# Kernel optimization log

Hardware: AMD Instinct MI355X
Metric: run time of the kernel (lower is better)

Reference implementation:

```python
import jax, jax.numpy as jnp
import numpy as np

SEQ, B, D_IN, D_H = 1024, 64, 256, 256


def setup_inputs() -> dict:
    key = jax.random.key(0)
    ks = jax.random.split(key, 9)
    scale = 1.0 / np.sqrt(D_IN + D_H)
    inputs = jax.random.normal(ks[0], (SEQ, B, D_IN), dtype=jnp.float32)
    def lin(k):
        kw, kb = jax.random.split(k)
        W = jax.random.uniform(kw, (D_IN + D_H, D_H), jnp.float32, -scale, scale)
        b = jax.random.uniform(kb, (D_H,), jnp.float32, -scale, scale)
        return W, b
    Wf, bf = lin(ks[1])
    Wi, bi = lin(ks[2])
    Wg, bg = lin(ks[3])
    Wo, bo = lin(ks[4])
    return {"inputs": inputs, "Wf": Wf, "bf": bf, "Wi": Wi, "bi": bi,
            "Wg": Wg, "bg": bg, "Wo": Wo, "bo": bo}


def reference(inputs, Wf, bf, Wi, bi, Wg, bg, Wo, bo):
    B_ = inputs.shape[1]
    hx0 = jnp.zeros((B_, D_H), dtype=inputs.dtype)
    cx0 = jnp.zeros((B_, D_H), dtype=inputs.dtype)

    def step(carry, x):
        hx, cx = carry
        comb = jnp.concatenate([x, hx], axis=1)  # [B, D_IN + D_H]
        f = jax.nn.sigmoid(comb @ Wf + bf)
        i = jax.nn.sigmoid(comb @ Wi + bi)
        g = jnp.tanh(comb @ Wg + bg)
        o = jax.nn.sigmoid(comb @ Wo + bo)
        cx = f * cx + i * g
        hx = o * jnp.tanh(cx)
        return (hx, cx), hx

    (hx, cx), outputs = jax.lax.scan(step, (hx0, cx0), inputs)
    return outputs, hx, cx
```

## Files before the change

kernel.cpp:

```cpp
#include <hip/hip_runtime.h>
#include <hip/hip_bf16.h>


typedef _Float16 f16;
typedef _Float16 f16x4 __attribute__((ext_vector_type(4)));
typedef _Float16 f16x8 __attribute__((ext_vector_type(8)));
typedef float f32x4 __attribute__((ext_vector_type(4)));
typedef int i32x4 __attribute__((ext_vector_type(4)));

#define SEQ 1024
#define BATCH 64
#define DIN 256
#define DH 256
#define NCOL 1024

#define WXP_OFF   0u
#define WHQ_OFF   524288u
#define SCL_OFF   786432u
#define BIAS_OFF  790528u
#define HXS8_OFF  794624u
#define CXS_OFF   811008u
#define SMX_OFF   876544u
#define XP_OFF    880640u

__device__ __forceinline__ float fast_sigmoid(float x) {
  float e = __expf(-x);
  return __builtin_amdgcn_rcpf(1.0f + e);
}
__device__ __forceinline__ float fast_tanh(float x) {
  x = fminf(fmaxf(x, -15.0f), 15.0f);
  float e = __expf(2.0f * x);
  return (e - 1.0f) * __builtin_amdgcn_rcpf(e + 1.0f);
}
__device__ __forceinline__ void lds_barrier() {
  asm volatile("s_waitcnt lgkmcnt(0)\n\ts_barrier" ::: "memory");
}
__device__ __forceinline__ i32x4 MQ(i32x4 a, i32x4 b, i32x4 c) {
  return __builtin_amdgcn_mfma_i32_16x16x64_i8(a, b, c, 0, 0, 0);
}

__global__ void qlstm_prep(const float* __restrict__ Wf, const float* __restrict__ Wi,
                           const float* __restrict__ Wg, const float* __restrict__ Wo,
                           const float* __restrict__ bf_, const float* __restrict__ bi_,
                           const float* __restrict__ bg_, const float* __restrict__ bo_,
                           f16* __restrict__ Wxp, float* __restrict__ biasp,
                           int* __restrict__ smx) {
  int tid = blockIdx.x * 256 + threadIdx.x;
  if (tid < 4 * 256 * 256) {
    int g = tid >> 16;
    int rem = tid & 65535;
    int k = rem >> 8, n = rem & 255;
    const float* W = (g == 0) ? Wf : (g == 1) ? Wi : (g == 2) ? Wg : Wo;
    float v = W[k * 256 + n];
    int j = n * 4 + g;
    Wxp[((size_t)(k >> 3) * 1024 + j) * 8 + (k & 7)] = (f16)v;
  }
  if (tid < 1024) {
    int g = tid >> 8, n = tid & 255;
    const float* bb = (g == 0) ? bf_ : (g == 1) ? bi_ : (g == 2) ? bg_ : bo_;
    biasp[n * 4 + g] = bb[n];
    smx[tid] = 0;
  }
}

__global__ __launch_bounds__(256) void qlstm_prepmax(
    const float* __restrict__ Wf, const float* __restrict__ Wi,
    const float* __restrict__ Wg, const float* __restrict__ Wo,
    int* __restrict__ smx) {
  int bk = blockIdx.x;
  int g = bk & 3, r0 = (bk >> 2) * 32;
  int n = threadIdx.x;
  const float* W = (g == 0) ? Wf : (g == 1) ? Wi : (g == 2) ? Wg : Wo;
  float pm = 0.0f;
  for (int r = 0; r < 32; ++r)
    pm = fmaxf(pm, fabsf(W[(size_t)(256 + r0 + r) * 256 + n]));
  atomicMax(&smx[g * 256 + n], __float_as_int(pm));
}

__global__ __launch_bounds__(256) void qlstm_prepq(
    const float* __restrict__ Wf, const float* __restrict__ Wi,
    const float* __restrict__ Wg, const float* __restrict__ Wo,
    const int* __restrict__ smx, char* __restrict__ WhQ, float* __restrict__ scl) {
  int bk = blockIdx.x;
  int g = bk & 3, r = bk >> 2;
  int n = threadIdx.x;
  const float* W = (g == 0) ? Wf : (g == 1) ? Wi : (g == 2) ? Wg : Wo;
  float mx = __int_as_float(smx[g * 256 + n]);
  float s = (mx > 0.0f) ? mx * (1.0f / 127.0f) : 1.0f;
  float v = W[(size_t)(256 + r) * 256 + n];
  int q = (int)rintf(v * (1.0f / s));
  q = q > 127 ? 127 : (q < -127 ? -127 : q);
  int w = n >> 4, c = n & 15;
  int kt = r >> 6, kp = r & 63;
  int lane = (kp >> 4) * 16 + c, jj = kp & 15;
  WhQ[((size_t)((w * 16 + g * 4 + kt) * 64 + lane)) * 16 + jj] = (char)q;
  if (r == 0) scl[g * 256 + n] = s * (1.0f / 127.0f);
}

__global__ __launch_bounds__(256) void qlstm_xproj(
    const float* __restrict__ X, const f16* __restrict__ Wxp,
    const float* __restrict__ biasp, f16* __restrict__ Xp2) {
  __shared__ f16 As[128][72];
  __shared__ f16 Bs[8 * 128 * 8];

  int tid = threadIdx.x;
  int tm = blockIdx.x, tn = blockIdx.y;
  int wave = tid >> 6, lane = tid & 63;
  int qm = (wave & 1) * 64, qn = (wave >> 1) * 64;
  int lm = lane & 15, lk = lane >> 4;

  f32x4 acc[4][4];
#pragma unroll
  for (int a = 0; a < 4; ++a)
#pragma unroll
    for (int b = 0; b < 4; ++b) acc[a][b] = (f32x4)0.0f;

  for (int k0 = 0; k0 < 256; k0 += 64) {
    {
      int r = tid >> 1, c0 = (tid & 1) * 32;
      const float4* src = (const float4*)(X + (size_t)(tm * 128 + r) * 256 + k0 + c0);
#pragma unroll
      for (int i = 0; i < 8; ++i) {
        float4 v = src[i];
        f16x4 pk = {(f16)v.x, (f16)v.y, (f16)v.z, (f16)v.w};
        *(f16x4*)&As[r][c0 + i * 4] = pk;
      }
    }
    {
#pragma unroll
      for (int it = 0; it < 4; ++it) {
        int idx = it * 256 + tid;
        int kgi = idx >> 7, n = idx & 127;
        ((uint4*)Bs)[idx] =
            *(const uint4*)(Wxp + (((size_t)(k0 >> 3) + kgi) * 1024 + tn * 128 + n) * 8);
      }
    }
    __syncthreads();
#pragma unroll
    for (int ks = 0; ks < 2; ++ks) {
      f16x8 af[4], bfr[4];
#pragma unroll
      for (int mi = 0; mi < 4; ++mi)
        af[mi] = *(const f16x8*)&As[qm + mi * 16 + lm][ks * 32 + lk * 8];
#pragma unroll
      for (int ni = 0; ni < 4; ++ni)
        bfr[ni] = *(const f16x8*)&Bs[(((ks * 4 + lk) * 128) + qn + ni * 16 + lm) * 8];
#pragma unroll
      for (int mi = 0; mi < 4; ++mi)
#pragma unroll
        for (int ni = 0; ni < 4; ++ni)
          acc[mi][ni] = __builtin_amdgcn_mfma_f32_16x16x32_f16(af[mi], bfr[ni],
                                                               acc[mi][ni], 0, 0, 0);
    }
    __syncthreads();
  }
  int m0 = tm * 128 + qm, j0 = tn * 128 + qn;
#pragma unroll
  for (int mi = 0; mi < 4; ++mi)
#pragma unroll
    for (int ni = 0; ni < 4; ++ni) {
      int j = j0 + ni * 16 + lm;
      float bv = biasp[j];
#pragma unroll
      for (int r = 0; r < 4; ++r) {
        int m = m0 + mi * 16 + lk * 4 + r;
        Xp2[(size_t)m * 1024 + j] = (f16)(acc[mi][ni][r] + bv);
      }
    }
}

__global__ __launch_bounds__(1024, 4) void qlstm_seq(
    const f16* __restrict__ Xp2, const i32x4* __restrict__ WhQ,
    const float* __restrict__ scl,
    float* __restrict__ out, char* __restrict__ hxs8, float* __restrict__ cxs,
    float* __restrict__ hxout, float* __restrict__ cxout, int t0, int t1) {
  __shared__ char hxq[2][256];

  int tid = threadIdx.x;
  int wv = tid >> 6, lane = tid & 63, c = lane & 15;
  int b = blockIdx.x;
  int h = wv * 16 + c;

  i32x4 wq[4][4];
  {
    const i32x4* wp = WhQ + (size_t)(wv * 16) * 64 + lane;
#pragma unroll
    for (int g = 0; g < 4; ++g)
#pragma unroll
      for (int kt = 0; kt < 4; ++kt) wq[g][kt] = wp[(g * 4 + kt) * 64];
  }
  float sc[4];
#pragma unroll
  for (int g = 0; g < 4; ++g) sc[g] = scl[g * 256 + h];

  int par0 = t0 & 1;
  if (tid < 16) {
    uint4 v;
    if (t0 == 0) v = uint4{0u, 0u, 0u, 0u};
    else v = ((const uint4*)(hxs8 + (size_t)b * 256))[tid];
    *(uint4*)(&hxq[par0][tid * 16]) = v;
  }
  float cx = (t0 != 0) ? cxs[(size_t)b * 256 + h] : 0.0f;

  __syncthreads();

  int koff = (lane >> 4) << 4;
  float hv = 0.0f;
  for (int t = t0; t < t1; ++t) {
    int par = t & 1, parn = par ^ 1;
    const char* hp = &hxq[par][0];

    uint2 xr = *(const uint2*)(Xp2 + (((size_t)(t - t0) * BATCH + b) * 256 + h) * 4);

    i32x4 a0 = *(const i32x4*)(hp + koff);
    i32x4 a1 = *(const i32x4*)(hp + 64 + koff);
    i32x4 a2 = *(const i32x4*)(hp + 128 + koff);
    i32x4 a3 = *(const i32x4*)(hp + 192 + koff);

    i32x4 acc0{}, acc1{}, acc2{}, acc3{};
    acc0 = MQ(a0, wq[0][0], acc0); acc1 = MQ(a0, wq[1][0], acc1);
    acc2 = MQ(a0, wq[2][0], acc2); acc3 = MQ(a0, wq[3][0], acc3);
    acc0 = MQ(a1, wq[0][1], acc0); acc1 = MQ(a1, wq[1][1], acc1);
    acc2 = MQ(a1, wq[2][1], acc2); acc3 = MQ(a1, wq[3][1], acc3);
    acc0 = MQ(a2, wq[0][2], acc0); acc1 = MQ(a2, wq[1][2], acc1);
    acc2 = MQ(a2, wq[2][2], acc2); acc3 = MQ(a2, wq[3][2], acc3);
    acc0 = MQ(a3, wq[0][3], acc0); acc1 = MQ(a3, wq[1][3], acc1);
    acc2 = MQ(a3, wq[2][3], acc2); acc3 = MQ(a3, wq[3][3], acc3);

    f16x4 xh = __builtin_bit_cast(f16x4, xr);
    float p0 = fmaf((float)acc0[0], sc[0], (float)xh[0]);
    float p1 = fmaf((float)acc1[0], sc[1], (float)xh[1]);
    float p2 = fmaf((float)acc2[0], sc[2], (float)xh[2]);
    float p3 = fmaf((float)acc3[0], sc[3], (float)xh[3]);

    float vf = fast_sigmoid(p0);
    float vi = fast_sigmoid(p1);
    float vg = fast_tanh(p2);
    float vo = fast_sigmoid(p3);
    cx = fmaf(vf, cx, vi * vg);
    hv = vo * fast_tanh(cx);

    if (lane < 16) {
      hxq[parn][h] = (char)(int)rintf(hv * 127.0f);
      out[((size_t)t * BATCH + b) * 256 + h] = hv;
    }
    lds_barrier();
  }

  if (tid < 16)
    ((uint4*)(hxs8 + (size_t)b * 256))[tid] = *(const uint4*)(&hxq[t1 & 1][tid * 16]);
  if (lane < 16) {
    cxs[(size_t)b * 256 + h] = cx;
    if (t1 == SEQ) {
      hxout[(size_t)b * 256 + h] = hv;
      cxout[(size_t)b * 256 + h] = cx;
    }
  }
}

extern "C" void kernel_launch(void* const* d_in, const int* in_sizes, int n_in,
                              void* d_out, int out_size, void* d_ws, size_t ws_size,
                              hipStream_t stream) {
  const float* X  = (const float*)d_in[0];
  const float* Wf = (const float*)d_in[1]; const float* bf_ = (const float*)d_in[2];
  const float* Wi = (const float*)d_in[3]; const float* bi_ = (const float*)d_in[4];
  const float* Wg = (const float*)d_in[5]; const float* bg_ = (const float*)d_in[6];
  const float* Wo = (const float*)d_in[7]; const float* bo_ = (const float*)d_in[8];
  float* out = (float*)d_out;

  char* ws = (char*)d_ws;
  f16*   Wxp   = (f16*)(ws + WXP_OFF);
  char*  WhQ   = (char*)(ws + WHQ_OFF);
  float* scl   = (float*)(ws + SCL_OFF);
  float* biasp = (float*)(ws + BIAS_OFF);
  char*  hxs8  = (char*)(ws + HXS8_OFF);
  float* cxs   = (float*)(ws + CXS_OFF);
  int*   smx   = (int*)(ws + SMX_OFF);
  f16*   Xp2   = (f16*)(ws + XP_OFF);

  size_t avail = (ws_size > XP_OFF) ? (ws_size - XP_OFF) : 0;
  int Tc = SEQ;
  while (Tc > 2 && (size_t)Tc * BATCH * NCOL * 2 > avail) Tc >>= 1;

  qlstm_prep<<<1024, 256, 0, stream>>>(Wf, Wi, Wg, Wo, bf_, bi_, bg_, bo_,
                                       Wxp, biasp, smx);
  qlstm_prepmax<<<32, 256, 0, stream>>>(Wf, Wi, Wg, Wo, smx);
  qlstm_prepq<<<1024, 256, 0, stream>>>(Wf, Wi, Wg, Wo, smx, WhQ, scl);

  float* hxout = out + (size_t)SEQ * BATCH * DH;
  float* cxout = hxout + BATCH * DH;

  for (int t0 = 0; t0 < SEQ; t0 += Tc) {
    dim3 g1(Tc * BATCH / 128, NCOL / 128);
    qlstm_xproj<<<g1, 256, 0, stream>>>(X + (size_t)t0 * BATCH * DIN, Wxp, biasp, Xp2);
    qlstm_seq<<<BATCH, 1024, 0, stream>>>(Xp2, (const i32x4*)WhQ, scl, out, hxs8, cxs,
                                          hxout, cxout, t0, t0 + Tc);
  }
}
```

Measured before the change: 1.161 ms.

## Restructure input projection to load X once per block, fuse weight-scale prep kernels

The input-projection GEMM now loads and converts each 128-row X tile once into a padded LDS buffer covering the full K=256, then loops over all 8 output column tiles, staging full-K weight tiles in dynamic LDS. This replaces the 2D grid where each block reloaded X per column tile. The weight max-reduction and int8 quantization kernels are merged into one kernel that reduces in shared memory instead of using global atomics, and tanh drops its clamp and uses a cheaper formula. The trade-offs are fewer xproj blocks (lower parallelism), about 128KB of LDS per block, and possible tanh edge behavior for large inputs.

```diff
diff --git a/kernel.cpp b/kernel.cpp
--- a/kernel.cpp
+++ b/kernel.cpp
@@ -20,17 +20,17 @@
 #define BIAS_OFF  790528u
 #define HXS8_OFF  794624u
 #define CXS_OFF   811008u
-#define SMX_OFF   876544u
-#define XP_OFF    880640u
+#define XP_OFF    876544u
+
+#define XPROJ_LDS 131584
 
 __device__ __forceinline__ float fast_sigmoid(float x) {
   float e = __expf(-x);
   return __builtin_amdgcn_rcpf(1.0f + e);
 }
 __device__ __forceinline__ float fast_tanh(float x) {
-  x = fminf(fmaxf(x, -15.0f), 15.0f);
   float e = __expf(2.0f * x);
-  return (e - 1.0f) * __builtin_amdgcn_rcpf(e + 1.0f);
+  return fmaf(-2.0f, __builtin_amdgcn_rcpf(e + 1.0f), 1.0f);
 }
 __device__ __forceinline__ void lds_barrier() {
   asm volatile("s_waitcnt lgkmcnt(0)\n\ts_barrier" ::: "memory");
@@ -43,8 +43,7 @@
                            const float* __restrict__ Wg, const float* __restrict__ Wo,
                            const float* __restrict__ bf_, const float* __restrict__ bi_,
                            const float* __restrict__ bg_, const float* __restrict__ bo_,
-                           f16* __restrict__ Wxp, float* __restrict__ biasp,
-                           int* __restrict__ smx) {
+                           f16* __restrict__ Wxp, float* __restrict__ biasp) {
   int tid = blockIdx.x * 256 + threadIdx.x;
   if (tid < 4 * 256 * 256) {
     int g = tid >> 16;
@@ -59,114 +58,118 @@
     int g = tid >> 8, n = tid & 255;
     const float* bb = (g == 0) ? bf_ : (g == 1) ? bi_ : (g == 2) ? bg_ : bo_;
     biasp[n * 4 + g] = bb[n];
-    smx[tid] = 0;
-  }
-}
-
-__global__ __launch_bounds__(256) void qlstm_prepmax(
+  }
+}
+
+__global__ __launch_bounds__(1024) void qlstm_prepq(
     const float* __restrict__ Wf, const float* __restrict__ Wi,
     const float* __restrict__ Wg, const float* __restrict__ Wo,
-    int* __restrict__ smx) {
-  int bk = blockIdx.x;
-  int g = bk & 3, r0 = (bk >> 2) * 32;
-  int n = threadIdx.x;
+    char* __restrict__ WhQ, float* __restrict__ scl) {
+  __shared__ float red[4][256];
+  int g = blockIdx.x;
+  int tid = threadIdx.x, q = tid >> 8, n = tid & 255;
   const float* W = (g == 0) ? Wf : (g == 1) ? Wi : (g == 2) ? Wg : Wo;
+
   float pm = 0.0f;
-  for (int r = 0; r < 32; ++r)
-    pm = fmaxf(pm, fabsf(W[(size_t)(256 + r0 + r) * 256 + n]));
-  atomicMax(&smx[g * 256 + n], __float_as_int(pm));
-}
-
-__global__ __launch_bounds__(256) void qlstm_prepq(
-    const float* __restrict__ Wf, const float* __restrict__ Wi,
-    const float* __restrict__ Wg, const float* __restrict__ Wo,
-    const int* __restrict__ smx, char* __restrict__ WhQ, float* __restrict__ scl) {
-  int bk = blockIdx.x;
-  int g = bk & 3, r = bk >> 2;
-  int n = threadIdx.x;
-  const float* W = (g == 0) ? Wf : (g == 1) ? Wi : (g == 2) ? Wg : Wo;
-  float mx = __int_as_float(smx[g * 256 + n]);
+  for (int r = 0; r < 64; ++r)
+    pm = fmaxf(pm, fabsf(W[(size_t)(256 + q * 64 + r) * 256 + n]));
+  red[q][n] = pm;
+  __syncthreads();
+  float mx = fmaxf(fmaxf(red[0][n], red[1][n]), fmaxf(red[2][n], red[3][n]));
   float s = (mx > 0.0f) ? mx * (1.0f / 127.0f) : 1.0f;
-  float v = W[(size_t)(256 + r) * 256 + n];
-  int q = (int)rintf(v * (1.0f / s));
-  q = q > 127 ? 127 : (q < -127 ? -127 : q);
+  float inv = 1.0f / s;
+
   int w = n >> 4, c = n & 15;
-  int kt = r >> 6, kp = r & 63;
-  int lane = (kp >> 4) * 16 + c, jj = kp & 15;
-  WhQ[((size_t)((w * 16 + g * 4 + kt) * 64 + lane)) * 16 + jj] = (char)q;
-  if (r == 0) scl[g * 256 + n] = s * (1.0f / 127.0f);
+  for (int rr = 0; rr < 64; ++rr) {
+    int r = q * 64 + rr;
+    float v = W[(size_t)(256 + r) * 256 + n];
+    int qv = (int)rintf(v * inv);
+    qv = qv > 127 ? 127 : (qv < -127 ? -127 : qv);
+    int kt = r >> 6, kp = r & 63;
+    int lane = (kp >> 4) * 16 + c, jj = kp & 15;
+    WhQ[((size_t)((w * 16 + g * 4 + kt) * 64 + lane)) * 16 + jj] = (char)qv;
+  }
+  if (q == 0) scl[g * 256 + n] = s * (1.0f / 127.0f);
 }
 
 __global__ __launch_bounds__(256) void qlstm_xproj(
     const float* __restrict__ X, const f16* __restrict__ Wxp,
     const float* __restrict__ biasp, f16* __restrict__ Xp2) {
-  __shared__ f16 As[128][72];
-  __shared__ f16 Bs[8 * 128 * 8];
+  extern __shared__ char smem[];
+  f16* As = (f16*)smem;
+  f16* Bs = (f16*)(smem + 66048);
 
   int tid = threadIdx.x;
-  int tm = blockIdx.x, tn = blockIdx.y;
+  int tm = blockIdx.x;
   int wave = tid >> 6, lane = tid & 63;
   int qm = (wave & 1) * 64, qn = (wave >> 1) * 64;
   int lm = lane & 15, lk = lane >> 4;
 
-  f32x4 acc[4][4];
-#pragma unroll
-  for (int a = 0; a < 4; ++a)
-#pragma unroll
-    for (int b = 0; b < 4; ++b) acc[a][b] = (f32x4)0.0f;
-
-  for (int k0 = 0; k0 < 256; k0 += 64) {
+  {
+    int r = tid >> 1, c0 = (tid & 1) * 128;
+    const float4* src = (const float4*)(X + (size_t)(tm * 128 + r) * 256 + c0);
+#pragma unroll
+    for (int i = 0; i < 32; ++i) {
+      float4 v = src[i];
+      f16x4 pk = {(f16)v.x, (f16)v.y, (f16)v.z, (f16)v.w};
+      *(f16x4*)&As[r * 258 + c0 + i * 4] = pk;
+    }
+  }
+
+  for (int tn = 0; tn < 8; ++tn) {
+    __syncthreads();
     {
-      int r = tid >> 1, c0 = (tid & 1) * 32;
-      const float4* src = (const float4*)(X + (size_t)(tm * 128 + r) * 256 + k0 + c0);
-#pragma unroll
-      for (int i = 0; i < 8; ++i) {
-        float4 v = src[i];
-        f16x4 pk = {(f16)v.x, (f16)v.y, (f16)v.z, (f16)v.w};
-        *(f16x4*)&As[r][c0 + i * 4] = pk;
+#pragma unroll
+      for (int it = 0; it < 16; ++it) {
+        int idx = it * 256 + tid;
+        int kg = idx >> 7, n = idx & 127;
+        ((uint4*)Bs)[idx] =
+            *(const uint4*)(Wxp + ((size_t)kg * 1024 + tn * 128 + n) * 8);
       }
     }
-    {
-#pragma unroll
-      for (int it = 0; it < 4; ++it) {
-        int idx = it * 256 + tid;
-        int kgi = idx >> 7, n = idx & 127;
-        ((uint4*)Bs)[idx] =
-            *(const uint4*)(Wxp + (((size_t)(k0 >> 3) + kgi) * 1024 + tn * 128 + n) * 8);
+    __syncthreads();
+
+    f32x4 acc[4][4];
+#pragma unroll
+    for (int a = 0; a < 4; ++a)
+#pragma unroll
+      for (int b = 0; b < 4; ++b) acc[a][b] = (f32x4)0.0f;
+
+#pragma unroll
+    for (int k0 = 0; k0 < 256; k0 += 64) {
+#pragma unroll
+      for (int ks = 0; ks < 2; ++ks) {
+        f16x8 af[4], bfr[4];
+        int kgab = (k0 >> 3) + ks * 4 + lk;
+#pragma unroll
+        for (int mi = 0; mi < 4; ++mi)
+          af[mi] = *(const f16x8*)&As[(qm + mi * 16 + lm) * 258 + k0 + ks * 32 + lk * 8];
+#pragma unroll
+        for (int ni = 0; ni < 4; ++ni)
+          bfr[ni] = *(const f16x8*)&Bs[((size_t)kgab * 128 + qn + ni * 16 + lm) * 8];
+#pragma unroll
+        for (int mi = 0; mi < 4; ++mi)
+#pragma unroll
+          for (int ni = 0; ni < 4; ++ni)
+            acc[mi][ni] = __builtin_amdgcn_mfma_f32_16x16x32_f16(af[mi], bfr[ni],
+                                                                 acc[mi][ni], 0, 0, 0);
       }
     }
-    __syncthreads();
-#pragma unroll
-    for (int ks = 0; ks < 2; ++ks) {
-      f16x8 af[4], bfr[4];
-#pragma unroll
-      for (int mi = 0; mi < 4; ++mi)
-        af[mi] = *(const f16x8*)&As[qm + mi * 16 + lm][ks * 32 + lk * 8];
-#pragma unroll
-      for (int ni = 0; ni < 4; ++ni)
-        bfr[ni] = *(const f16x8*)&Bs[(((ks * 4 + lk) * 128) + qn + ni * 16 + lm) * 8];
-#pragma unroll
-      for (int mi = 0; mi < 4; ++mi)
-#pragma unroll
-        for (int ni = 0; ni < 4; ++ni)
-          acc[mi][ni] = __builtin_amdgcn_mfma_f32_16x16x32_f16(af[mi], bfr[ni],
-                                                               acc[mi][ni], 0, 0, 0);
-    }
-    __syncthreads();
-  }
-  int m0 = tm * 128 + qm, j0 = tn * 128 + qn;
-#pragma unroll
-  for (int mi = 0; mi < 4; ++mi)
-#pragma unroll
-    for (int ni = 0; ni < 4; ++ni) {
-      int j = j0 + ni * 16 + lm;
-      float bv = biasp[j];
-#pragma unroll
-      for (int r = 0; r < 4; ++r) {
-        int m = m0 + mi * 16 + lk * 4 + r;
-        Xp2[(size_t)m * 1024 + j] = (f16)(acc[mi][ni][r] + bv);
+
+    int m0 = tm * 128 + qm, j0 = tn * 128 + qn;
+#pragma unroll
+    for (int mi = 0; mi < 4; ++mi)
+#pragma unroll
+      for (int ni = 0; ni < 4; ++ni) {
+        int j = j0 + ni * 16 + lm;
+        float bv = biasp[j];
+#pragma unroll
+        for (int r = 0; r < 4; ++r) {
+          int m = m0 + mi * 16 + lk * 4 + r;
+          Xp2[(size_t)m * 1024 + j] = (f16)(acc[mi][ni][r] + bv);
+        }
       }
-    }
+  }
 }
 
 __global__ __launch_bounds__(1024, 4) void qlstm_seq(
@@ -275,7 +278,6 @@
   float* biasp = (float*)(ws + BIAS_OFF);
   char*  hxs8  = (char*)(ws + HXS8_OFF);
   float* cxs   = (float*)(ws + CXS_OFF);
-  int*   smx   = (int*)(ws + SMX_OFF);
   f16*   Xp2   = (f16*)(ws + XP_OFF);
 
   size_t avail = (ws_size > XP_OFF) ? (ws_size - XP_OFF) : 0;
@@ -283,16 +285,19 @@
   while (Tc > 2 && (size_t)Tc * BATCH * NCOL * 2 > avail) Tc >>= 1;
 
   qlstm_prep<<<1024, 256, 0, stream>>>(Wf, Wi, Wg, Wo, bf_, bi_, bg_, bo_,
-                                       Wxp, biasp, smx);
-  qlstm_prepmax<<<32, 256, 0, stream>>>(Wf, Wi, Wg, Wo, smx);
-  qlstm_prepq<<<1024, 256, 0, stream>>>(Wf, Wi, Wg, Wo, smx, WhQ, scl);
+                                       Wxp, biasp);
+  qlstm_prepq<<<4, 1024, 0, stream>>>(Wf, Wi, Wg, Wo, WhQ, scl);
+
+  (void)hipFuncSetAttribute((const void*)qlstm_xproj,
+                            hipFuncAttributeMaxDynamicSharedMemorySize,
+                            XPROJ_LDS);
 
   float* hxout = out + (size_t)SEQ * BATCH * DH;
   float* cxout = hxout + BATCH * DH;
 
   for (int t0 = 0; t0 < SEQ; t0 += Tc) {
-    dim3 g1(Tc * BATCH / 128, NCOL / 128);
-    qlstm_xproj<<<g1, 256, 0, stream>>>(X + (size_t)t0 * BATCH * DIN, Wxp, biasp, Xp2);
+    qlstm_xproj<<<Tc * 64 / 128, 256, XPROJ_LDS, stream>>>(
+        X + (size_t)t0 * BATCH * DIN, Wxp, biasp, Xp2);
     qlstm_seq<<<BATCH, 1024, 0, stream>>>(Xp2, (const i32x4*)WhQ, scl, out, hxs8, cxs,
                                           hxout, cxout, t0, t0 + Tc);
   }
```

New measurement: 1.169 ms. Within noise of the previous version (+0.7%).
